# Kernel tuning notes

Measured on AMD Instinct MI355X. Metric: run time of the kernel, lower is better.

Reference implementation:

```python
import jax, jax.numpy as jnp
import numpy as np

B, D, E, H, C, TOPK = 4096, 768, 16, 768, 1000, 4

def setup_inputs() -> dict:
    key = jax.random.key(0)
    ks = jax.random.split(key, 4)
    s_in = 1.0 / np.sqrt(D)
    return {
        'features': jax.random.normal(ks[0], (B, D), dtype=jnp.float32),
        'router_w': jax.random.normal(ks[1], (D, E), dtype=jnp.float32) * s_in,
        'router_b': jnp.zeros((E,), jnp.float32),
        'ln_g': jnp.ones((E, D), jnp.float32),
        'ln_b': jnp.zeros((E, D), jnp.float32),
        'w1': jax.random.normal(ks[2], (E, D, H), dtype=jnp.float32) * s_in,
        'b1': jnp.zeros((E, H), jnp.float32),
        'w2': jax.random.normal(ks[3], (E, H, C), dtype=jnp.float32) * (1.0 / np.sqrt(H)),
        'b2': jnp.zeros((E, C), jnp.float32),
    }

def reference(features, router_w, router_b, ln_g, ln_b, w1, b1, w2, b2):
    # router
    gate_logits = features @ router_w + router_b          # [B,E]
    gate_probs = jax.nn.softmax(gate_logits, axis=-1)
    topk_vals, topk_idx = jax.lax.top_k(gate_probs, TOPK)  # [B,K]
    topk_vals = topk_vals / jnp.sum(topk_vals, axis=-1, keepdims=True)

    # all experts computed densely: LayerNorm (per-expert affine) -> Linear -> GELU -> Linear
    mu = jnp.mean(features, axis=-1, keepdims=True)
    var = jnp.mean((features - mu) ** 2, axis=-1, keepdims=True)
    xn = (features - mu) / jnp.sqrt(var + 1e-5)            # [B,D]
    y = xn[:, None, :] * ln_g[None, :, :] + ln_b[None, :, :]  # [B,E,D]
    h = jax.nn.gelu(jnp.einsum('bed,edh->beh', y, w1) + b1[None], approximate=False)  # [B,E,H]
    all_logits = jnp.einsum('beh,ehc->bec', h, w2) + b2[None]  # [B,E,C]

    # top-k gather + weighted softmax mixture
    selected = jnp.take_along_axis(all_logits, topk_idx[:, :, None], axis=1)  # [B,K,C]
    market_probs = jnp.sum(topk_vals[:, :, None] * jax.nn.softmax(selected, axis=-1), axis=1)  # [B,C]
    all_probs = jax.nn.softmax(jnp.transpose(all_logits, (1, 0, 2)), axis=-1)  # [E,B,C]
    return market_probs, all_probs, gate_probs
```

## Files before the change

### kernel.cpp

```cpp
#include <hip/hip_runtime.h>
#include <hip/hip_bf16.h>
#include <cmath>

#define B_ 4096
#define D_ 768
#define E_ 16
#define H_ 768
#define C_ 1000
#define CP_ 1024
#define K_ 768

typedef __bf16 bf16_t;
typedef __bf16 bf16x8 __attribute__((ext_vector_type(8)));
typedef float f32x4 __attribute__((ext_vector_type(4)));

__device__ __forceinline__ void async_lds16(const void* g, void* l) {
  __builtin_amdgcn_global_load_lds(
      (const __attribute__((address_space(1))) void*)g,
      (__attribute__((address_space(3))) void*)l, 16, 0, 0);
}

__global__ __launch_bounds__(256) void k_router_ln(
    const float* __restrict__ feat, const float* __restrict__ rw,
    const float* __restrict__ rb, float* __restrict__ gate_out,
    int* __restrict__ tk_idx, float* __restrict__ tk_val,
    bf16_t* __restrict__ xn) {
  int w = threadIdx.x >> 6, lane = threadIdx.x & 63;
  int b = blockIdx.x * 4 + w;
  float acc[E_];
#pragma unroll
  for (int e = 0; e < E_; ++e) acc[e] = 0.f;
  const float* frow = feat + (size_t)b * D_;
  float v[D_ / 64];
  float s = 0.f, sq = 0.f;
#pragma unroll
  for (int it = 0; it < D_ / 64; ++it) {
    int d = it * 64 + lane;
    float f = frow[d];
    v[it] = f; s += f; sq += f * f;
    const float4* r4 = reinterpret_cast<const float4*>(rw + (size_t)d * E_);
    float4 q0 = r4[0], q1 = r4[1], q2 = r4[2], q3 = r4[3];
    acc[0]  += f * q0.x; acc[1]  += f * q0.y; acc[2]  += f * q0.z; acc[3]  += f * q0.w;
    acc[4]  += f * q1.x; acc[5]  += f * q1.y; acc[6]  += f * q1.z; acc[7]  += f * q1.w;
    acc[8]  += f * q2.x; acc[9]  += f * q2.y; acc[10] += f * q2.z; acc[11] += f * q2.w;
    acc[12] += f * q3.x; acc[13] += f * q3.y; acc[14] += f * q3.z; acc[15] += f * q3.w;
  }
#pragma unroll
  for (int off = 32; off; off >>= 1) { s += __shfl_xor(s, off); sq += __shfl_xor(sq, off); }
  float mu = s * (1.f / D_);
  float var = sq * (1.f / D_) - mu * mu;
  float rs = rsqrtf(var + 1e-5f);
  bf16_t* o = xn + (size_t)b * D_;
#pragma unroll
  for (int it = 0; it < D_ / 64; ++it)
    o[it * 64 + lane] = (bf16_t)((v[it] - mu) * rs);
#pragma unroll
  for (int e = 0; e < E_; ++e) {
#pragma unroll
    for (int off = 32; off; off >>= 1) acc[e] += __shfl_xor(acc[e], off);
    acc[e] += rb[e];
  }
  if (lane == 0) {
    float mx = acc[0];
#pragma unroll
    for (int e = 1; e < E_; ++e) mx = fmaxf(mx, acc[e]);
    float p[E_]; float ps = 0.f;
#pragma unroll
    for (int e = 0; e < E_; ++e) { p[e] = expf(acc[e] - mx); ps += p[e]; }
    float inv = 1.f / ps;
    float* go = gate_out + (size_t)b * E_;
#pragma unroll
    for (int e = 0; e < E_; ++e) { p[e] *= inv; go[e] = p[e]; }
    float lg[E_];
#pragma unroll
    for (int e = 0; e < E_; ++e) lg[e] = acc[e];
    int idx4[4]; float v4[4]; float vs = 0.f;
#pragma unroll
    for (int k = 0; k < 4; ++k) {
      int bi = 0; float bv = -1e30f;
#pragma unroll
      for (int e = 0; e < E_; ++e) { if (lg[e] > bv) { bv = lg[e]; bi = e; } }
      idx4[k] = bi; v4[k] = p[bi]; vs += p[bi]; lg[bi] = -1e30f;
    }
    float nv = 1.f / vs;
#pragma unroll
    for (int k = 0; k < 4; ++k) { tk_idx[b * 4 + k] = idx4[k]; tk_val[b * 4 + k] = v4[k] * nv; }
  }
}

__global__ __launch_bounds__(256) void k_bias_init(const float* __restrict__ b1,
                                                   float* __restrict__ bias1) {
  int i = blockIdx.x * 256 + threadIdx.x;
  bias1[i] = b1[i];
}

__global__ void k_tw1(const float* __restrict__ w1, const float* __restrict__ lng,
                      const float* __restrict__ lnb, bf16_t* __restrict__ w1T,
                      float* __restrict__ bias1) {
  __shared__ float t[32][33];
  __shared__ float br[8][33];
  int e = blockIdx.z, dT = blockIdx.y * 32, hT = blockIdx.x * 32;
  int tx = threadIdx.x, ty = threadIdx.y;
  const float* w1e = w1 + (size_t)e * D_ * H_;
  const float* ge = lng + (size_t)e * D_;
  const float* lb = lnb + (size_t)e * D_;
  float bsum = 0.f;
#pragma unroll
  for (int r = 0; r < 4; ++r) {
    int d = dT + ty + r * 8;
    float val = w1e[(size_t)d * H_ + hT + tx];
    t[ty + r * 8][tx] = val * ge[d];
    bsum += lb[d] * val;
  }
  br[ty][tx] = bsum;
  __syncthreads();
  bf16_t* o = w1T + (size_t)e * H_ * D_;
#pragma unroll
  for (int r = 0; r < 4; ++r) {
    int h = hT + ty + r * 8;
    o[(size_t)h * D_ + dT + tx] = (bf16_t)t[tx][ty + r * 8];
  }
  if (ty == 0) {
    float a = 0.f;
#pragma unroll
    for (int z = 0; z < 8; ++z) a += br[z][tx];
    atomicAdd(&bias1[(size_t)e * H_ + hT + tx], a);
  }
}

__global__ void k_tw2(const float* __restrict__ w2, bf16_t* __restrict__ w2T) {
  __shared__ float t[32][33];
  int e = blockIdx.z, hT = blockIdx.y * 32, cT = blockIdx.x * 32;
  int tx = threadIdx.x, ty = threadIdx.y;
  const float* w2e = w2 + (size_t)e * H_ * C_;
#pragma unroll
  for (int r = 0; r < 4; ++r) {
    int h = hT + ty + r * 8, c = cT + tx;
    t[ty + r * 8][tx] = (c < C_) ? w2e[(size_t)h * C_ + c] : 0.f;
  }
  __syncthreads();
  bf16_t* o = w2T + (size_t)e * CP_ * H_;
#pragma unroll
  for (int r = 0; r < 4; ++r) {
    int c = cT + ty + r * 8;
    o[(size_t)c * H_ + hT + tx] = (bf16_t)t[tx][ty + r * 8];
  }
}

template <int MODE>
__global__ __launch_bounds__(512, 2) void k_gemm256(
    const bf16_t* __restrict__ Abase, size_t aStride,
    const bf16_t* __restrict__ Bt, int Np,
    const float* __restrict__ bias,
    bf16_t* __restrict__ outb, float* __restrict__ outf) {
  __shared__ __attribute__((aligned(16))) bf16_t smbuf[2][2][256 * 64];
  int id = blockIdx.x;
  int xcd = id & 7, seq = id >> 3;
  int e, m0, n0;
  if (MODE == 0) {
    int m = seq / 6, rr = seq % 6;
    e = xcd * 2 + rr / 3;
    m0 = m * 256;
    n0 = (rr % 3) * 256;
  } else {
    e = xcd * 2 + (seq >> 6);
    int rr = seq & 63;
    m0 = (rr >> 2) * 256;
    n0 = (rr & 3) * 256;
  }
  const bf16_t* A = Abase + (size_t)e * aStride + (size_t)m0 * K_;
  const bf16_t* Bp = Bt + ((size_t)e * Np + n0) * K_;

  int tid = threadIdx.x;
  int lane = tid & 63;
  int wid = tid >> 6;
  int wm = wid >> 2, wn = wid & 3;
  int fr = lane & 15, hi = lane >> 4;
  int sw0 = (hi ^ (fr & 7)) * 8;

  int srow = tid >> 3;
  int scg = (tid & 7) ^ (srow & 7);
  const bf16_t* asrc = A + (size_t)srow * K_ + scg * 8;
  const bf16_t* bsrc = Bp + (size_t)srow * K_ + scg * 8;

  f32x4 acc[8][4];
#pragma unroll
  for (int i = 0; i < 8; ++i)
#pragma unroll
    for (int j = 0; j < 4; ++j) acc[i][j] = f32x4{0.f, 0.f, 0.f, 0.f};

  auto STAGE = [&](int kt, int nb) {
    bf16_t* ad = &smbuf[nb][0][tid * 8];
    bf16_t* bd = &smbuf[nb][1][tid * 8];
    const bf16_t* as = asrc + kt * 64;
    const bf16_t* bs = bsrc + kt * 64;
#pragma unroll
    for (int s = 0; s < 4; ++s) {
      async_lds16(as + (size_t)s * 64 * K_, ad + s * 4096);
      async_lds16(bs + (size_t)s * 64 * K_, bd + s * 4096);
    }
  };

  bf16x8 af[4][2], bfr[2][2];
  auto COMPUTE = [&](int cur) {
    const bf16_t* Ala = &smbuf[cur][0][(wm * 128 + fr) * 64];
    const bf16_t* Bla = &smbuf[cur][1][(wn * 64 + fr) * 64];
#pragma unroll
    for (int q = 0; q < 4; ++q) {
      const int mq = q >> 1;
      const int nq = (q == 1 || q == 2);
      if (q == 0 || q == 2) {
#pragma unroll
        for (int i = 0; i < 4; ++i)
#pragma unroll
          for (int ks = 0; ks < 2; ++ks)
            af[i][ks] = *(const bf16x8*)&Ala[(mq * 64 + i * 16) * 64 + (sw0 ^ (ks * 32))];
      }
      if (q != 2) {
#pragma unroll
        for (int j = 0; j < 2; ++j)
#pragma unroll
          for (int ks = 0; ks < 2; ++ks)
            bfr[j][ks] = *(const bf16x8*)&Bla[(nq * 32 + j * 16) * 64 + (sw0 ^ (ks * 32))];
      }
      __builtin_amdgcn_s_barrier();
      __builtin_amdgcn_s_setprio(1);
#pragma unroll
      for (int i = 0; i < 4; ++i)
#pragma unroll
        for (int j = 0; j < 2; ++j)
#pragma unroll
          for (int ks = 0; ks < 2; ++ks)
            acc[mq * 4 + i][nq * 2 + j] = __builtin_amdgcn_mfma_f32_16x16x32_bf16(
                af[i][ks], bfr[j][ks], acc[mq * 4 + i][nq * 2 + j], 0, 0, 0);
      __builtin_amdgcn_s_setprio(0);
      __builtin_amdgcn_s_barrier();
    }
  };

  constexpr int NKT = K_ / 64;
  STAGE(0, 0);
  for (int t = 0; t < NKT - 1; ++t) {
    STAGE(t + 1, (t + 1) & 1);
    asm volatile("s_waitcnt vmcnt(8)" ::: "memory");
    __builtin_amdgcn_s_barrier();
    COMPUTE(t & 1);
  }
  asm volatile("s_waitcnt vmcnt(0)" ::: "memory");
  __builtin_amdgcn_s_barrier();
  COMPUTE((NKT - 1) & 1);

  int rb = hi * 4;
  int cl = fr;
#pragma unroll
  for (int i = 0; i < 8; ++i) {
#pragma unroll
    for (int j = 0; j < 4; ++j) {
      int n = n0 + wn * 64 + j * 16 + cl;
      if (MODE == 0) {
        float bs = bias[(size_t)e * H_ + n];
#pragma unroll
        for (int r = 0; r < 4; ++r) {
          int m = m0 + wm * 128 + i * 16 + rb + r;
          float vv = acc[i][j][r] + bs;
          vv = 0.5f * vv * (1.f + erff(vv * 0.70710678118654752f));
          outb[((size_t)e * B_ + m) * H_ + n] = (bf16_t)vv;
        }
      } else if (MODE == 1) {
        float bs = (n < C_) ? bias[(size_t)e * C_ + n] : 0.f;
#pragma unroll
        for (int r = 0; r < 4; ++r) {
          int m = m0 + wm * 128 + i * 16 + rb + r;
          outb[((size_t)e * B_ + m) * CP_ + n] = (bf16_t)(acc[i][j][r] + bs);
        }
      } else {
        if (n < C_) {
          float bs = bias[(size_t)e * C_ + n];
#pragma unroll
          for (int r = 0; r < 4; ++r) {
            int m = m0 + wm * 128 + i * 16 + rb + r;
            outf[((size_t)e * B_ + m) * C_ + n] = acc[i][j][r] + bs;
          }
        }
      }
    }
  }
}

__global__ __launch_bounds__(256) void k_softmax_b(const bf16_t* __restrict__ lg,
                                                   float* __restrict__ out1) {
  int w = threadIdx.x >> 6, lane = threadIdx.x & 63;
  size_t r = (size_t)blockIdx.x * 4 + w;
  const bf16_t* row = lg + r * CP_;
  float f[2][8];
  float mx = -1e30f;
#pragma unroll
  for (int it = 0; it < 2; ++it) {
    int ch = it * 64 + lane;
    bf16x8 x = *(const bf16x8*)(row + ch * 8);
    if (ch < 125) {
#pragma unroll
      for (int q = 0; q < 8; ++q) { f[it][q] = (float)x[q]; mx = fmaxf(mx, f[it][q]); }
    }
  }
#pragma unroll
  for (int off = 32; off; off >>= 1) mx = fmaxf(mx, __shfl_xor(mx, off));
  float s = 0.f;
#pragma unroll
  for (int it = 0; it < 2; ++it) {
    int ch = it * 64 + lane;
    if (ch < 125) {
#pragma unroll
      for (int q = 0; q < 8; ++q) { f[it][q] = __expf(f[it][q] - mx); s += f[it][q]; }
    }
  }
#pragma unroll
  for (int off = 32; off; off >>= 1) s += __shfl_xor(s, off);
  float inv = 1.f / s;
  float* orow = out1 + r * C_;
#pragma unroll
  for (int it = 0; it < 2; ++it) {
    int ch = it * 64 + lane;
    if (ch < 125) {
      float4 a = make_float4(f[it][0] * inv, f[it][1] * inv, f[it][2] * inv, f[it][3] * inv);
      float4 b = make_float4(f[it][4] * inv, f[it][5] * inv, f[it][6] * inv, f[it][7] * inv);
      *(float4*)(orow + ch * 8) = a;
      *(float4*)(orow + ch * 8 + 4) = b;
    }
  }
}

__global__ __launch_bounds__(256) void k_softmax(float* __restrict__ p) {
  int w = threadIdx.x >> 6, lane = threadIdx.x & 63;
  size_t r = (size_t)blockIdx.x * 4 + w;
  float* row = p + r * C_;
  float4* row4 = reinterpret_cast<float4*>(row);
  const int n4 = C_ / 4;
  float4 v[4];
  float mx = -1e30f;
#pragma unroll
  for (int i = 0; i < 4; ++i) {
    int idx = i * 64 + lane;
    if (idx < n4) {
      v[i] = row4[idx];
      mx = fmaxf(mx, fmaxf(fmaxf(v[i].x, v[i].y), fmaxf(v[i].z, v[i].w)));
    }
  }
#pragma unroll
  for (int off = 32; off; off >>= 1) mx = fmaxf(mx, __shfl_xor(mx, off));
  float s = 0.f;
#pragma unroll
  for (int i = 0; i < 4; ++i) {
    int idx = i * 64 + lane;
    if (idx < n4) {
      v[i].x = __expf(v[i].x - mx); v[i].y = __expf(v[i].y - mx);
      v[i].z = __expf(v[i].z - mx); v[i].w = __expf(v[i].w - mx);
      s += v[i].x + v[i].y + v[i].z + v[i].w;
    }
  }
#pragma unroll
  for (int off = 32; off; off >>= 1) s += __shfl_xor(s, off);
  float inv = 1.f / s;
#pragma unroll
  for (int i = 0; i < 4; ++i) {
    int idx = i * 64 + lane;
    if (idx < n4) {
      v[i].x *= inv; v[i].y *= inv; v[i].z *= inv; v[i].w *= inv;
      row4[idx] = v[i];
    }
  }
}

__global__ __launch_bounds__(256) void k_market(const float* __restrict__ allp,
                                                const int* __restrict__ tki,
                                                const float* __restrict__ tkv,
                                                float* __restrict__ out0) {
  int b = blockIdx.y;
  int c = blockIdx.x * 256 + threadIdx.x;
  if (c >= C_) return;
  const int* ix = tki + (size_t)b * 4;
  const float* vv = tkv + (size_t)b * 4;
  float s = 0.f;
#pragma unroll
  for (int k = 0; k < 4; ++k)
    s += vv[k] * allp[((size_t)ix[k] * B_ + b) * C_ + c];
  out0[(size_t)b * C_ + c] = s;
}

extern "C" void kernel_launch(void* const* d_in, const int* in_sizes, int n_in,
                              void* d_out, int out_size, void* d_ws, size_t ws_size,
                              hipStream_t stream) {
  const float* feat = (const float*)d_in[0];
  const float* rw   = (const float*)d_in[1];
  const float* rb   = (const float*)d_in[2];
  const float* lng  = (const float*)d_in[3];
  const float* lnb  = (const float*)d_in[4];
  const float* w1   = (const float*)d_in[5];
  const float* b1   = (const float*)d_in[6];
  const float* w2   = (const float*)d_in[7];
  const float* b2   = (const float*)d_in[8];

  float* out0 = (float*)d_out;
  float* out1 = out0 + (size_t)B_ * C_;
  float* out2 = out1 + (size_t)E_ * B_ * C_;

  char* ws = (char*)d_ws;
  size_t off = 0;
  auto take = [&](size_t bytes) -> void* {
    void* p = ws + off;
    off += (bytes + 255) & ~(size_t)255;
    return p;
  };
  bf16_t* xn   = (bf16_t*)take((size_t)B_ * D_ * 2);
  bf16_t* w1T  = (bf16_t*)take((size_t)E_ * H_ * D_ * 2);
  bf16_t* w2T  = (bf16_t*)take((size_t)E_ * CP_ * H_ * 2);
  float* bias1 = (float*)take((size_t)E_ * H_ * 4);
  int* tki     = (int*)take((size_t)B_ * 4 * 4);
  float* tkv   = (float*)take((size_t)B_ * 4 * 4);
  bf16_t* Hact = (bf16_t*)take((size_t)E_ * B_ * H_ * 2);
  size_t logit_bytes = (size_t)E_ * B_ * CP_ * 2;
  bool use_b16_logits = (off + logit_bytes) <= ws_size;
  bf16_t* logitsB = use_b16_logits ? (bf16_t*)take(logit_bytes) : nullptr;

  k_router_ln<<<B_ / 4, 256, 0, stream>>>(feat, rw, rb, out2, tki, tkv, xn);
  k_bias_init<<<E_ * H_ / 256, 256, 0, stream>>>(b1, bias1);
  k_tw1<<<dim3(24, 24, E_), dim3(32, 8), 0, stream>>>(w1, lng, lnb, w1T, bias1);
  k_tw2<<<dim3(32, 24, E_), dim3(32, 8), 0, stream>>>(w2, w2T);
  k_gemm256<0><<<E_ * 16 * 3, 512, 0, stream>>>(xn, 0, w1T, H_, bias1, Hact, nullptr);
  if (use_b16_logits) {
    k_gemm256<1><<<E_ * 16 * 4, 512, 0, stream>>>(Hact, (size_t)B_ * H_, w2T, CP_, b2, logitsB, nullptr);
    k_softmax_b<<<(E_ * B_) / 4, 256, 0, stream>>>(logitsB, out1);
  } else {
    k_gemm256<2><<<E_ * 16 * 4, 512, 0, stream>>>(Hact, (size_t)B_ * H_, w2T, CP_, b2, nullptr, out1);
    k_softmax<<<(E_ * B_) / 4, 256, 0, stream>>>(out1);
  }
  k_market<<<dim3(4, B_), 256, 0, stream>>>(out1, tki, tkv, out0);
}
```

Measured before the change: 703.4 us.

## Fuse second expert GEMM with row softmax in full-row tile kernel

Replaces the second GEMM plus separate softmax pass with one kernel where each block computes a 64-row by full-1024-column logit tile and does the row softmax in registers, using LDS for cross-wave max/sum reductions. This removes the round trip of bf16 (or fp32) logits through global memory and one kernel launch. In exchange the tile shape is narrow in M with a large B stage per K step (64KB double-buffered), and the final stores are scattered scalar writes rather than vectorised, which may reduce GEMM efficiency.

```diff
diff --git a/kernel.cpp b/kernel.cpp
--- a/kernel.cpp
+++ b/kernel.cpp
@@ -287,88 +287,156 @@
   }
 }
 
-__global__ __launch_bounds__(256) void k_softmax_b(const bf16_t* __restrict__ lg,
-                                                   float* __restrict__ out1) {
-  int w = threadIdx.x >> 6, lane = threadIdx.x & 63;
-  size_t r = (size_t)blockIdx.x * 4 + w;
-  const bf16_t* row = lg + r * CP_;
-  float f[2][8];
-  float mx = -1e30f;
-#pragma unroll
-  for (int it = 0; it < 2; ++it) {
-    int ch = it * 64 + lane;
-    bf16x8 x = *(const bf16x8*)(row + ch * 8);
-    if (ch < 125) {
-#pragma unroll
-      for (int q = 0; q < 8; ++q) { f[it][q] = (float)x[q]; mx = fmaxf(mx, f[it][q]); }
-    }
-  }
-#pragma unroll
-  for (int off = 32; off; off >>= 1) mx = fmaxf(mx, __shfl_xor(mx, off));
-  float s = 0.f;
-#pragma unroll
-  for (int it = 0; it < 2; ++it) {
-    int ch = it * 64 + lane;
-    if (ch < 125) {
-#pragma unroll
-      for (int q = 0; q < 8; ++q) { f[it][q] = __expf(f[it][q] - mx); s += f[it][q]; }
-    }
-  }
-#pragma unroll
-  for (int off = 32; off; off >>= 1) s += __shfl_xor(s, off);
-  float inv = 1.f / s;
-  float* orow = out1 + r * C_;
-#pragma unroll
-  for (int it = 0; it < 2; ++it) {
-    int ch = it * 64 + lane;
-    if (ch < 125) {
-      float4 a = make_float4(f[it][0] * inv, f[it][1] * inv, f[it][2] * inv, f[it][3] * inv);
-      float4 b = make_float4(f[it][4] * inv, f[it][5] * inv, f[it][6] * inv, f[it][7] * inv);
-      *(float4*)(orow + ch * 8) = a;
-      *(float4*)(orow + ch * 8 + 4) = b;
-    }
-  }
-}
-
-__global__ __launch_bounds__(256) void k_softmax(float* __restrict__ p) {
-  int w = threadIdx.x >> 6, lane = threadIdx.x & 63;
-  size_t r = (size_t)blockIdx.x * 4 + w;
-  float* row = p + r * C_;
-  float4* row4 = reinterpret_cast<float4*>(row);
-  const int n4 = C_ / 4;
-  float4 v[4];
-  float mx = -1e30f;
-#pragma unroll
-  for (int i = 0; i < 4; ++i) {
-    int idx = i * 64 + lane;
-    if (idx < n4) {
-      v[i] = row4[idx];
-      mx = fmaxf(mx, fmaxf(fmaxf(v[i].x, v[i].y), fmaxf(v[i].z, v[i].w)));
-    }
-  }
-#pragma unroll
-  for (int off = 32; off; off >>= 1) mx = fmaxf(mx, __shfl_xor(mx, off));
-  float s = 0.f;
-#pragma unroll
-  for (int i = 0; i < 4; ++i) {
-    int idx = i * 64 + lane;
-    if (idx < n4) {
-      v[i].x = __expf(v[i].x - mx); v[i].y = __expf(v[i].y - mx);
-      v[i].z = __expf(v[i].z - mx); v[i].w = __expf(v[i].w - mx);
-      s += v[i].x + v[i].y + v[i].z + v[i].w;
-    }
-  }
-#pragma unroll
-  for (int off = 32; off; off >>= 1) s += __shfl_xor(s, off);
-  float inv = 1.f / s;
-#pragma unroll
-  for (int i = 0; i < 4; ++i) {
-    int idx = i * 64 + lane;
-    if (idx < n4) {
-      v[i].x *= inv; v[i].y *= inv; v[i].z *= inv; v[i].w *= inv;
-      row4[idx] = v[i];
-    }
-  }
+__global__ __launch_bounds__(512, 2) void k_gemm2_sm(
+    const bf16_t* __restrict__ Hact, const bf16_t* __restrict__ w2T,
+    const float* __restrict__ b2, float* __restrict__ out1) {
+  __shared__ __attribute__((aligned(16))) bf16_t Bsm[2][32768];
+  __shared__ __attribute__((aligned(16))) bf16_t Asm[2][2048];
+  int id = blockIdx.x;
+  int xcd = id & 7, seq = id >> 3;
+  int e = xcd * 2 + (seq >> 6);
+  int m0 = (seq & 63) * 64;
+  const bf16_t* A = Hact + ((size_t)e * B_ + m0) * K_;
+  const bf16_t* Bp = w2T + (size_t)e * CP_ * K_;
+
+  int tid = threadIdx.x;
+  int lane = tid & 63, wn = tid >> 6;
+  int fr = lane & 15, hi = lane >> 4;
+
+  f32x4 acc[4][8];
+#pragma unroll
+  for (int i = 0; i < 4; ++i)
+#pragma unroll
+    for (int j = 0; j < 8; ++j) acc[i][j] = f32x4{0.f, 0.f, 0.f, 0.f};
+
+  const bf16_t* bbase = Bp + (size_t)tid * K_;
+  int ga = tid & 255;
+  int arow = ga & 63, akg = ga >> 6;
+  const bf16_t* abase = A + (size_t)arow * K_ + akg * 8;
+
+  auto STAGE = [&](int kt, int nb) {
+    bf16_t* bd = &Bsm[nb][0];
+#pragma unroll
+    for (int s = 0; s < 8; ++s) {
+      const bf16_t* src = bbase + (size_t)((s & 1) * 512) * K_ + (s >> 1) * 8 + kt * 32;
+      async_lds16(src, bd + (s * 512 + tid) * 8);
+    }
+    async_lds16(abase + kt * 32, &Asm[nb][ga * 8]);
+  };
+
+  auto COMPUTE = [&](int cur) {
+    bf16x8 af[4], bf[8];
+#pragma unroll
+    for (int i = 0; i < 4; ++i)
+      af[i] = *(const bf16x8*)&Asm[cur][(hi * 64 + i * 16 + fr) * 8];
+#pragma unroll
+    for (int j = 0; j < 8; ++j)
+      bf[j] = *(const bf16x8*)&Bsm[cur][(hi * 1024 + wn * 128 + j * 16 + fr) * 8];
+    __builtin_amdgcn_s_setprio(1);
+#pragma unroll
+    for (int i = 0; i < 4; ++i)
+#pragma unroll
+      for (int j = 0; j < 8; ++j)
+        acc[i][j] = __builtin_amdgcn_mfma_f32_16x16x32_bf16(af[i], bf[j], acc[i][j], 0, 0, 0);
+    __builtin_amdgcn_s_setprio(0);
+  };
+
+  constexpr int NKT = K_ / 32;
+  STAGE(0, 0);
+  for (int t = 0; t < NKT - 1; ++t) {
+    STAGE(t + 1, (t + 1) & 1);
+    asm volatile("s_waitcnt vmcnt(9)" ::: "memory");
+    __builtin_amdgcn_s_barrier();
+    COMPUTE(t & 1);
+    __builtin_amdgcn_s_barrier();
+  }
+  asm volatile("s_waitcnt vmcnt(0)" ::: "memory");
+  __builtin_amdgcn_s_barrier();
+  COMPUTE((NKT - 1) & 1);
+  __syncthreads();
+
+  int colb[8]; bool val[8]; float bc[8];
+#pragma unroll
+  for (int j = 0; j < 8; ++j) {
+    int col = wn * 128 + j * 16 + fr;
+    colb[j] = col;
+    val[j] = (col < C_);
+    bc[j] = val[j] ? b2[(size_t)e * C_ + col] : 0.f;
+  }
+#pragma unroll
+  for (int i = 0; i < 4; ++i)
+#pragma unroll
+    for (int j = 0; j < 8; ++j)
+#pragma unroll
+      for (int r = 0; r < 4; ++r) acc[i][j][r] += bc[j];
+
+  float* red = (float*)&Asm[0][0];
+  float rm[4][4];
+#pragma unroll
+  for (int i = 0; i < 4; ++i)
+#pragma unroll
+    for (int r = 0; r < 4; ++r) {
+      float m = -1e30f;
+#pragma unroll
+      for (int j = 0; j < 8; ++j) m = val[j] ? fmaxf(m, acc[i][j][r]) : m;
+#pragma unroll
+      for (int off = 1; off < 16; off <<= 1) m = fmaxf(m, __shfl_xor(m, off));
+      rm[i][r] = m;
+    }
+  if (fr == 0) {
+#pragma unroll
+    for (int i = 0; i < 4; ++i)
+#pragma unroll
+      for (int r = 0; r < 4; ++r) red[wn * 64 + i * 16 + hi * 4 + r] = rm[i][r];
+  }
+  __syncthreads();
+#pragma unroll
+  for (int i = 0; i < 4; ++i)
+#pragma unroll
+    for (int r = 0; r < 4; ++r) {
+      int row = i * 16 + hi * 4 + r;
+      float m = red[row];
+#pragma unroll
+      for (int w = 1; w < 8; ++w) m = fmaxf(m, red[w * 64 + row]);
+      rm[i][r] = m;
+    }
+  __syncthreads();
+  float rs[4][4];
+#pragma unroll
+  for (int i = 0; i < 4; ++i)
+#pragma unroll
+    for (int r = 0; r < 4; ++r) {
+      float s = 0.f;
+#pragma unroll
+      for (int j = 0; j < 8; ++j) {
+        float p = val[j] ? __expf(acc[i][j][r] - rm[i][r]) : 0.f;
+        acc[i][j][r] = p; s += p;
+      }
+#pragma unroll
+      for (int off = 1; off < 16; off <<= 1) s += __shfl_xor(s, off);
+      rs[i][r] = s;
+    }
+  if (fr == 0) {
+#pragma unroll
+    for (int i = 0; i < 4; ++i)
+#pragma unroll
+      for (int r = 0; r < 4; ++r) red[wn * 64 + i * 16 + hi * 4 + r] = rs[i][r];
+  }
+  __syncthreads();
+#pragma unroll
+  for (int i = 0; i < 4; ++i)
+#pragma unroll
+    for (int r = 0; r < 4; ++r) {
+      int row = i * 16 + hi * 4 + r;
+      float s = red[row];
+#pragma unroll
+      for (int w = 1; w < 8; ++w) s += red[w * 64 + row];
+      float inv = 1.f / s;
+      float* orow = out1 + ((size_t)e * B_ + m0 + row) * C_;
+#pragma unroll
+      for (int j = 0; j < 8; ++j)
+        if (val[j]) orow[colb[j]] = acc[i][j][r] * inv;
+    }
 }
 
 __global__ __launch_bounds__(256) void k_market(const float* __restrict__ allp,
@@ -418,21 +486,12 @@
   int* tki     = (int*)take((size_t)B_ * 4 * 4);
   float* tkv   = (float*)take((size_t)B_ * 4 * 4);
   bf16_t* Hact = (bf16_t*)take((size_t)E_ * B_ * H_ * 2);
-  size_t logit_bytes = (size_t)E_ * B_ * CP_ * 2;
-  bool use_b16_logits = (off + logit_bytes) <= ws_size;
-  bf16_t* logitsB = use_b16_logits ? (bf16_t*)take(logit_bytes) : nullptr;
 
   k_router_ln<<<B_ / 4, 256, 0, stream>>>(feat, rw, rb, out2, tki, tkv, xn);
   k_bias_init<<<E_ * H_ / 256, 256, 0, stream>>>(b1, bias1);
   k_tw1<<<dim3(24, 24, E_), dim3(32, 8), 0, stream>>>(w1, lng, lnb, w1T, bias1);
   k_tw2<<<dim3(32, 24, E_), dim3(32, 8), 0, stream>>>(w2, w2T);
   k_gemm256<0><<<E_ * 16 * 3, 512, 0, stream>>>(xn, 0, w1T, H_, bias1, Hact, nullptr);
-  if (use_b16_logits) {
-    k_gemm256<1><<<E_ * 16 * 4, 512, 0, stream>>>(Hact, (size_t)B_ * H_, w2T, CP_, b2, logitsB, nullptr);
-    k_softmax_b<<<(E_ * B_) / 4, 256, 0, stream>>>(logitsB, out1);
-  } else {
-    k_gemm256<2><<<E_ * 16 * 4, 512, 0, stream>>>(Hact, (size_t)B_ * H_, w2T, CP_, b2, nullptr, out1);
-    k_softmax<<<(E_ * B_) / 4, 256, 0, stream>>>(out1);
-  }
+  k_gemm2_sm<<<E_ * 64, 512, 0, stream>>>(Hact, w2T, b2, out1);
   k_market<<<dim3(4, B_), 256, 0, stream>>>(out1, tki, tkv, out0);
 }
```

Result: slower. 1.035 ms (+47.2%).

## Fuse market mixture into bf16 softmax and merge bias init into W1 transpose

Applied to the files above, without the earlier changes.

The per-expert softmax kernel now loops over all 16 experts for each batch row. It writes all_probs and accumulates the top-k weighted mixture in registers, so the separate k_market pass that re-read the fp32 probabilities is removed. The W1 transpose kernel now walks the whole D dimension per block and writes bias1 directly, which drops the bias-init kernel and the atomics. The trade-off is fewer blocks: 1024 for the softmax and 384 for the transpose, which lowers parallelism and latency hiding.

```diff
diff --git a/kernel.cpp b/kernel.cpp
--- a/kernel.cpp
+++ b/kernel.cpp
@@ -88,43 +88,42 @@
   }
 }
 
-__global__ __launch_bounds__(256) void k_bias_init(const float* __restrict__ b1,
-                                                   float* __restrict__ bias1) {
-  int i = blockIdx.x * 256 + threadIdx.x;
-  bias1[i] = b1[i];
-}
-
-__global__ void k_tw1(const float* __restrict__ w1, const float* __restrict__ lng,
-                      const float* __restrict__ lnb, bf16_t* __restrict__ w1T,
-                      float* __restrict__ bias1) {
+__global__ void k_tw1b(const float* __restrict__ w1, const float* __restrict__ lng,
+                       const float* __restrict__ lnb, const float* __restrict__ b1,
+                       bf16_t* __restrict__ w1T, float* __restrict__ bias1) {
   __shared__ float t[32][33];
   __shared__ float br[8][33];
-  int e = blockIdx.z, dT = blockIdx.y * 32, hT = blockIdx.x * 32;
+  int hT = blockIdx.x * 32, e = blockIdx.y;
   int tx = threadIdx.x, ty = threadIdx.y;
   const float* w1e = w1 + (size_t)e * D_ * H_;
   const float* ge = lng + (size_t)e * D_;
   const float* lb = lnb + (size_t)e * D_;
+  bf16_t* o = w1T + (size_t)e * H_ * D_;
   float bsum = 0.f;
-#pragma unroll
-  for (int r = 0; r < 4; ++r) {
-    int d = dT + ty + r * 8;
-    float val = w1e[(size_t)d * H_ + hT + tx];
-    t[ty + r * 8][tx] = val * ge[d];
-    bsum += lb[d] * val;
+  for (int r0 = 0; r0 < D_ / 32; ++r0) {
+#pragma unroll
+    for (int s = 0; s < 4; ++s) {
+      int dl = ty + s * 8;
+      int d = r0 * 32 + dl;
+      float val = w1e[(size_t)d * H_ + hT + tx];
+      t[dl][tx] = val * ge[d];
+      bsum += lb[d] * val;
+    }
+    __syncthreads();
+#pragma unroll
+    for (int s = 0; s < 4; ++s) {
+      int hl = ty + s * 8;
+      o[(size_t)(hT + hl) * D_ + r0 * 32 + tx] = (bf16_t)t[tx][hl];
+    }
+    __syncthreads();
   }
   br[ty][tx] = bsum;
   __syncthreads();
-  bf16_t* o = w1T + (size_t)e * H_ * D_;
-#pragma unroll
-  for (int r = 0; r < 4; ++r) {
-    int h = hT + ty + r * 8;
-    o[(size_t)h * D_ + dT + tx] = (bf16_t)t[tx][ty + r * 8];
-  }
   if (ty == 0) {
     float a = 0.f;
 #pragma unroll
     for (int z = 0; z < 8; ++z) a += br[z][tx];
-    atomicAdd(&bias1[(size_t)e * H_ + hT + tx], a);
+    bias1[(size_t)e * H_ + hT + tx] = b1[(size_t)e * H_ + hT + tx] + a;
   }
 }
 
@@ -287,45 +286,71 @@
   }
 }
 
-__global__ __launch_bounds__(256) void k_softmax_b(const bf16_t* __restrict__ lg,
-                                                   float* __restrict__ out1) {
+__global__ __launch_bounds__(256) void k_sm_market(
+    const bf16_t* __restrict__ lg, const int* __restrict__ tki,
+    const float* __restrict__ tkv, float* __restrict__ out1,
+    float* __restrict__ out0) {
   int w = threadIdx.x >> 6, lane = threadIdx.x & 63;
-  size_t r = (size_t)blockIdx.x * 4 + w;
-  const bf16_t* row = lg + r * CP_;
-  float f[2][8];
-  float mx = -1e30f;
-#pragma unroll
-  for (int it = 0; it < 2; ++it) {
-    int ch = it * 64 + lane;
-    bf16x8 x = *(const bf16x8*)(row + ch * 8);
-    if (ch < 125) {
-#pragma unroll
-      for (int q = 0; q < 8; ++q) { f[it][q] = (float)x[q]; mx = fmaxf(mx, f[it][q]); }
-    }
-  }
-#pragma unroll
-  for (int off = 32; off; off >>= 1) mx = fmaxf(mx, __shfl_xor(mx, off));
-  float s = 0.f;
+  int b = blockIdx.x * 4 + w;
+  const int* ixp = tki + (size_t)b * 4;
+  const float* vvp = tkv + (size_t)b * 4;
+  int i0 = ixp[0], i1 = ixp[1], i2 = ixp[2], i3 = ixp[3];
+  float v0 = vvp[0], v1 = vvp[1], v2 = vvp[2], v3 = vvp[3];
+  float mac[2][8];
+#pragma unroll
+  for (int it = 0; it < 2; ++it)
+#pragma unroll
+    for (int q = 0; q < 8; ++q) mac[it][q] = 0.f;
+#pragma unroll 2
+  for (int e = 0; e < E_; ++e) {
+    const bf16_t* row = lg + ((size_t)e * B_ + b) * CP_;
+    float f[2][8];
+    float mx = -1e30f;
+#pragma unroll
+    for (int it = 0; it < 2; ++it) {
+      int ch = it * 64 + lane;
+      bf16x8 x = *(const bf16x8*)(row + ch * 8);
+      if (ch < 125) {
+#pragma unroll
+        for (int q = 0; q < 8; ++q) { f[it][q] = (float)x[q]; mx = fmaxf(mx, f[it][q]); }
+      }
+    }
+#pragma unroll
+    for (int off = 32; off; off >>= 1) mx = fmaxf(mx, __shfl_xor(mx, off));
+    float s = 0.f;
+#pragma unroll
+    for (int it = 0; it < 2; ++it) {
+      int ch = it * 64 + lane;
+      if (ch < 125) {
+#pragma unroll
+        for (int q = 0; q < 8; ++q) { f[it][q] = __expf(f[it][q] - mx); s += f[it][q]; }
+      }
+    }
+#pragma unroll
+    for (int off = 32; off; off >>= 1) s += __shfl_xor(s, off);
+    float inv = 1.f / s;
+    float wg = (i0 == e ? v0 : 0.f) + (i1 == e ? v1 : 0.f) +
+               (i2 == e ? v2 : 0.f) + (i3 == e ? v3 : 0.f);
+    float* orow = out1 + ((size_t)e * B_ + b) * C_;
+#pragma unroll
+    for (int it = 0; it < 2; ++it) {
+      int ch = it * 64 + lane;
+      if (ch < 125) {
+        float p[8];
+#pragma unroll
+        for (int q = 0; q < 8; ++q) { p[q] = f[it][q] * inv; mac[it][q] += wg * p[q]; }
+        *(float4*)(orow + ch * 8)     = make_float4(p[0], p[1], p[2], p[3]);
+        *(float4*)(orow + ch * 8 + 4) = make_float4(p[4], p[5], p[6], p[7]);
+      }
+    }
+  }
+  float* mrow = out0 + (size_t)b * C_;
 #pragma unroll
   for (int it = 0; it < 2; ++it) {
     int ch = it * 64 + lane;
     if (ch < 125) {
-#pragma unroll
-      for (int q = 0; q < 8; ++q) { f[it][q] = __expf(f[it][q] - mx); s += f[it][q]; }
-    }
-  }
-#pragma unroll
-  for (int off = 32; off; off >>= 1) s += __shfl_xor(s, off);
-  float inv = 1.f / s;
-  float* orow = out1 + r * C_;
-#pragma unroll
-  for (int it = 0; it < 2; ++it) {
-    int ch = it * 64 + lane;
-    if (ch < 125) {
-      float4 a = make_float4(f[it][0] * inv, f[it][1] * inv, f[it][2] * inv, f[it][3] * inv);
-      float4 b = make_float4(f[it][4] * inv, f[it][5] * inv, f[it][6] * inv, f[it][7] * inv);
-      *(float4*)(orow + ch * 8) = a;
-      *(float4*)(orow + ch * 8 + 4) = b;
+      *(float4*)(mrow + ch * 8)     = make_float4(mac[it][0], mac[it][1], mac[it][2], mac[it][3]);
+      *(float4*)(mrow + ch * 8 + 4) = make_float4(mac[it][4], mac[it][5], mac[it][6], mac[it][7]);
     }
   }
 }
@@ -423,16 +448,15 @@
   bf16_t* logitsB = use_b16_logits ? (bf16_t*)take(logit_bytes) : nullptr;
 
   k_router_ln<<<B_ / 4, 256, 0, stream>>>(feat, rw, rb, out2, tki, tkv, xn);
-  k_bias_init<<<E_ * H_ / 256, 256, 0, stream>>>(b1, bias1);
-  k_tw1<<<dim3(24, 24, E_), dim3(32, 8), 0, stream>>>(w1, lng, lnb, w1T, bias1);
+  k_tw1b<<<dim3(24, E_), dim3(32, 8), 0, stream>>>(w1, lng, lnb, b1, w1T, bias1);
   k_tw2<<<dim3(32, 24, E_), dim3(32, 8), 0, stream>>>(w2, w2T);
   k_gemm256<0><<<E_ * 16 * 3, 512, 0, stream>>>(xn, 0, w1T, H_, bias1, Hact, nullptr);
   if (use_b16_logits) {
     k_gemm256<1><<<E_ * 16 * 4, 512, 0, stream>>>(Hact, (size_t)B_ * H_, w2T, CP_, b2, logitsB, nullptr);
-    k_softmax_b<<<(E_ * B_) / 4, 256, 0, stream>>>(logitsB, out1);
+    k_sm_market<<<B_ / 4, 256, 0, stream>>>(logitsB, tki, tkv, out1, out0);
   } else {
     k_gemm256<2><<<E_ * 16 * 4, 512, 0, stream>>>(Hact, (size_t)B_ * H_, w2T, CP_, b2, nullptr, out1);
     k_softmax<<<(E_ * B_) / 4, 256, 0, stream>>>(out1);
-  }
-  k_market<<<dim3(4, B_), 256, 0, stream>>>(out1, tki, tkv, out0);
-}
+    k_market<<<dim3(4, B_), 256, 0, stream>>>(out1, tki, tkv, out0);
+  }
+}
```

Measured after the change: 708.9 us. About the same (+0.8%).
